# Performance work log

Hardware: AMD Instinct MI355X
Metric: run time of the kernel (lower is better)

Reference implementation:

```python
import jax, jax.numpy as jnp
import numpy as np

B, Q, K, H = 8, 512, 512, 64
KEY_D, QUERY_D, VAL_D = 256, 256, 256

def setup_inputs() -> dict:
    key = jax.random.key(0)
    ks = jax.random.split(key, 6)
    return {
        "key": jax.random.normal(ks[0], (B, K, KEY_D), dtype=jnp.float32),
        "query": jax.random.normal(ks[1], (B, Q, QUERY_D), dtype=jnp.float32),
        "value": jax.random.normal(ks[2], (B, K, VAL_D), dtype=jnp.float32),
        "mask": jnp.zeros((B, Q, K), dtype=bool),
        "W_k": jax.random.normal(ks[3], (KEY_D, H), dtype=jnp.float32) / np.sqrt(KEY_D),
        "W_q": jax.random.normal(ks[4], (QUERY_D, H), dtype=jnp.float32) / np.sqrt(QUERY_D),
        "w_v": jax.random.normal(ks[5], (H,), dtype=jnp.float32) / np.sqrt(H),
    }

def reference(key, query, value, mask, W_k, W_q, w_v):
    q = query @ W_q                      # [B, Q, H]
    k = key @ W_k                        # [B, K, H]
    feats = jnp.tanh(q[:, :, None, :] + k[:, None, :, :])  # [B, Q, K, H]
    score = jnp.einsum('bqkh,h->bqk', feats, w_v)           # [B, Q, K]
    score = jnp.where(mask, -jnp.inf, score)
    attn = jax.nn.softmax(score, axis=-1)                   # [B, Q, K]
    return jnp.einsum('bqk,bkd->bqd', attn, value)          # [B, Q, VAL_D]
```

## Files before the change

kernel.cpp:

```cpp
#include <hip/hip_runtime.h>
#include <math.h>

#define NB 8
#define NQ 512
#define NK 512
#define NH 64
#define ND 256
#define QT 8

typedef float f32x2 __attribute__((ext_vector_type(2)));
typedef float f32x4 __attribute__((ext_vector_type(4)));

#define EXP2(x) __builtin_amdgcn_exp2f(x)
#define RCP(x)  __builtin_amdgcn_rcpf(x)
#define SCALE2 2.8853900817779268f
#define LOG2E  1.4426950408889634f

static __device__ __forceinline__ f32x2 sp2(float v) { return (f32x2){v, v}; }
static __device__ __forceinline__ f32x2 fma2(f32x2 a, f32x2 b, f32x2 c) {
    return __builtin_elementwise_fma(a, b, c);
}
static __device__ __forceinline__ f32x2 mk2(float x, float y) {
    return (f32x2){x, y};
}

__global__ __launch_bounds__(256, 4) void proj_kernel(
    const float* __restrict__ query, const float* __restrict__ key,
    const float* __restrict__ Wq, const float* __restrict__ Wk,
    float* __restrict__ Eq, float* __restrict__ Ekp)
{
    __shared__ __align__(16) float insT[ND][12];
    __shared__ float pacc[3][4][NH][2];
    const int t = threadIdx.x;
    const bool isK = blockIdx.x >= 512;
    const float* __restrict__ in = isK ? key : query;
    const float* __restrict__ W  = isK ? Wk : Wq;
    const int rowbase = (blockIdx.x & 511) * 8;

    {
        const int r = t & 7, c = (t >> 3) * 8;
        const float* src = in + (size_t)(rowbase + r) * ND + c;
        const f32x4 v0 = *(const f32x4*)src;
        const f32x4 v1 = *(const f32x4*)(src + 4);
        insT[c + 0][r] = v0.x; insT[c + 1][r] = v0.y;
        insT[c + 2][r] = v0.z; insT[c + 3][r] = v0.w;
        insT[c + 4][r] = v1.x; insT[c + 5][r] = v1.y;
        insT[c + 6][r] = v1.z; insT[c + 7][r] = v1.w;
    }
    __syncthreads();

    const int lane = t & 63;
    const int w    = t >> 6;
    const int d0   = w * 64;

    f32x2 acc[4] = {{0.f,0.f},{0.f,0.f},{0.f,0.f},{0.f,0.f}};
    for (int dd = 0; dd < 64; ++dd) {
        const int d = d0 + dd;
        const float wv = W[(size_t)d * NH + lane];
        const f32x4 rA = *(const f32x4*)&insT[d][0];
        const f32x4 rB = *(const f32x4*)&insT[d][4];
        acc[0] = fma2(mk2(rA.x, rA.y), sp2(wv), acc[0]);
        acc[1] = fma2(mk2(rA.z, rA.w), sp2(wv), acc[1]);
        acc[2] = fma2(mk2(rB.x, rB.y), sp2(wv), acc[2]);
        acc[3] = fma2(mk2(rB.z, rB.w), sp2(wv), acc[3]);
    }
    if (w > 0) {
        #pragma unroll
        for (int rp = 0; rp < 4; ++rp)
            *(f32x2*)&pacc[w - 1][rp][lane][0] = acc[rp];
    }
    __syncthreads();
    if (w == 0) {
        float e[8];
        #pragma unroll
        for (int rp = 0; rp < 4; ++rp) {
            f32x2 a = acc[rp];
            a += *(const f32x2*)&pacc[0][rp][lane][0];
            a += *(const f32x2*)&pacc[1][rp][lane][0];
            a += *(const f32x2*)&pacc[2][rp][lane][0];
            e[2 * rp] = a.x; e[2 * rp + 1] = a.y;
        }
        #pragma unroll
        for (int j = 0; j < 8; ++j) {
            const float x = fminf(fmaxf(e[j] * SCALE2, -30.f), 30.f);
            e[j] = EXP2(x);
        }
        if (!isK) {
            #pragma unroll
            for (int j = 0; j < 8; ++j)
                Eq[(size_t)(rowbase + j) * NH + lane] = e[j];
        } else {
            #pragma unroll
            for (int j = 0; j < 8; ++j) {
                const int g = rowbase + j;
                const int bb = g >> 9, kk = g & 511;
                Ekp[((size_t)bb * NH + lane) * NK + kk] = e[j];
            }
        }
    }
}

__global__ __launch_bounds__(512, 4) void attn_kernel(
    const float* __restrict__ Eq, const float* __restrict__ Ekp,
    const float* __restrict__ value, const unsigned char* __restrict__ mask,
    const float* __restrict__ w_v, float* __restrict__ out)
{
    __shared__ __align__(16) float qT[NH][4][4];
    __shared__ float w01[32];
    __shared__ __align__(16) float ps[QT][NK];
    __shared__ __align__(16) float reds[QT][8];
    __shared__ __align__(16) float pacc[3][4][ND];

    const int t    = threadIdx.x;
    const int lane = t & 63;
    const int w    = t >> 6;
    const int b    = blockIdx.x >> 6;
    const int q0   = (blockIdx.x & 63) * QT;

    {
        const int r = w, h = lane;
        const float e = Eq[(size_t)(b * NQ + q0 + r) * NH + h];
        qT[h][r >> 1][r & 1]       = e;
        qT[h][r >> 1][2 + (r & 1)] = w_v[h ^ 1] * e;
    }
    if (t < 32) w01[t] = w_v[2 * t] + w_v[2 * t + 1];
    float wl = w_v[lane];
    #pragma unroll
    for (int off = 32; off; off >>= 1) wl += __shfl_xor(wl, off, 64);
    const float wsumL = wl * LOG2E;
    __syncthreads();

    const int k = (w << 6) + lane;
    const float* __restrict__ ekc = Ekp + (size_t)b * NH * NK + k;

    f32x2 acc[4] = {{0.f,0.f},{0.f,0.f},{0.f,0.f},{0.f,0.f}};
    float eka[4];
    #pragma unroll
    for (int j = 0; j < 4; ++j) eka[j] = ekc[(size_t)j * NK];

    for (int hc = 0; hc < 16; ++hc) {
        const float ek0 = eka[0], ek1 = eka[1], ek2 = eka[2], ek3 = eka[3];
        if (hc < 15) {
            #pragma unroll
            for (int j = 0; j < 4; ++j)
                eka[j] = ekc[(size_t)(4 * (hc + 1) + j) * NK];
        }
        const f32x2 w2 = *(const f32x2*)&w01[2 * hc];
        const int hb = 4 * hc;
        #pragma unroll
        for (int rp = 0; rp < 4; ++rp) {
            const f32x4 g0 = *(const f32x4*)&qT[hb + 0][rp][0];
            const f32x4 g1 = *(const f32x4*)&qT[hb + 1][rp][0];
            const f32x4 g2 = *(const f32x4*)&qT[hb + 2][rp][0];
            const f32x4 g3 = *(const f32x4*)&qT[hb + 3][rp][0];
            const f32x2 t0 = mk2(g0.x, g0.y) * ek0;
            const f32x2 t1 = mk2(g1.x, g1.y) * ek1;
            const f32x2 ua = t0 + t1 + 1.0f;
            const f32x2 da = fma2(t0, t1, ua);
            f32x2 na = fma2(mk2(g0.z, g0.w), sp2(ek0), sp2(w2.x));
            na = fma2(mk2(g1.z, g1.w), sp2(ek1), na);
            const f32x2 t2 = mk2(g2.x, g2.y) * ek2;
            const f32x2 t3 = mk2(g3.x, g3.y) * ek3;
            const f32x2 ub = t2 + t3 + 1.0f;
            const f32x2 db = fma2(t2, t3, ub);
            f32x2 nb = fma2(mk2(g2.z, g2.w), sp2(ek2), sp2(w2.y));
            nb = fma2(mk2(g3.z, g3.w), sp2(ek3), nb);
            const f32x2 D = da * db;
            f32x2 N = na * db;
            N = fma2(nb, da, N);
            const f32x2 rD = mk2(RCP(D.x), RCP(D.y));
            acc[rp] = fma2(N, rD, acc[rp]);
        }
    }

    float p[8];
    {
        const unsigned char* __restrict__ mb =
            mask + (size_t)(b * NQ + q0) * NK + k;
        #pragma unroll
        for (int rp = 0; rp < 4; ++rp) {
            const f32x2 arg = fma2(acc[rp], sp2(-2.f * LOG2E), sp2(wsumL));
            p[2 * rp]     = mb[(size_t)(2 * rp) * NK]     ? -__builtin_inff() : arg.x;
            p[2 * rp + 1] = mb[(size_t)(2 * rp + 1) * NK] ? -__builtin_inff() : arg.y;
        }
        #pragma unroll
        for (int r = 0; r < 8; ++r) p[r] = EXP2(p[r]);
    }

    #pragma unroll
    for (int r = 0; r < 8; ++r) {
        float s = p[r];
        #pragma unroll
        for (int off = 32; off; off >>= 1) s += __shfl_xor(s, off, 64);
        if (lane == 0) reds[r][w] = s;
    }
    __syncthreads();
    #pragma unroll
    for (int r = 0; r < 8; ++r) {
        const f32x4 sa = *(const f32x4*)&reds[r][0];
        const f32x4 sb = *(const f32x4*)&reds[r][4];
        const float gsum = ((sa.x + sa.y) + (sa.z + sa.w)) +
                           ((sb.x + sb.y) + (sb.z + sb.w));
        ps[r][k] = p[r] * RCP(gsum);
    }
    __syncthreads();

    const int kq   = w >> 1;
    const int dh   = w & 1;
    const int dcol = dh * 128 + 2 * lane;
    f32x2 a[QT];
    #pragma unroll
    for (int r = 0; r < QT; ++r) a[r] = (f32x2){0.f, 0.f};

    const float* __restrict__ vb = value + ((size_t)b * NK + kq * 128) * ND + dcol;
    for (int kk = 0; kk < 128; kk += 4) {
        const int kbase = kq * 128 + kk;
        const f32x2 v0 = *(const f32x2*)&vb[(size_t)(kk + 0) * ND];
        const f32x2 v1 = *(const f32x2*)&vb[(size_t)(kk + 1) * ND];
        const f32x2 v2 = *(const f32x2*)&vb[(size_t)(kk + 2) * ND];
        const f32x2 v3 = *(const f32x2*)&vb[(size_t)(kk + 3) * ND];
        #pragma unroll
        for (int half = 0; half < 2; ++half) {
            #pragma unroll
            for (int rr = 0; rr < 4; ++rr) {
                const int r = half * 4 + rr;
                const f32x4 P = *(const f32x4*)&ps[r][kbase];
                a[r] = fma2(sp2(P.x), v0, a[r]);
                a[r] = fma2(sp2(P.y), v1, a[r]);
                a[r] = fma2(sp2(P.z), v2, a[r]);
                a[r] = fma2(sp2(P.w), v3, a[r]);
            }
        }
    }

    if (kq > 0) {
        #pragma unroll
        for (int r = 0; r < 4; ++r)
            *(f32x2*)&pacc[kq - 1][r][dcol] = a[r];
    }
    __syncthreads();
    if (kq == 0) {
        #pragma unroll
        for (int r = 0; r < 4; ++r) {
            f32x2 v = a[r];
            v += *(const f32x2*)&pacc[0][r][dcol];
            v += *(const f32x2*)&pacc[1][r][dcol];
            v += *(const f32x2*)&pacc[2][r][dcol];
            *(f32x2*)&out[(size_t)(b * NQ + q0 + r) * ND + dcol] = v;
        }
    }
    __syncthreads();
    if (kq > 0) {
        #pragma unroll
        for (int r = 0; r < 4; ++r)
            *(f32x2*)&pacc[kq - 1][r][dcol] = a[4 + r];
    }
    __syncthreads();
    if (kq == 0) {
        #pragma unroll
        for (int r = 0; r < 4; ++r) {
            f32x2 v = a[4 + r];
            v += *(const f32x2*)&pacc[0][r][dcol];
            v += *(const f32x2*)&pacc[1][r][dcol];
            v += *(const f32x2*)&pacc[2][r][dcol];
            *(f32x2*)&out[(size_t)(b * NQ + q0 + 4 + r) * ND + dcol] = v;
        }
    }
}

extern "C" void kernel_launch(void* const* d_in, const int* in_sizes, int n_in,
                              void* d_out, int out_size, void* d_ws, size_t ws_size,
                              hipStream_t stream) {
    const float* key   = (const float*)d_in[0];
    const float* query = (const float*)d_in[1];
    const float* value = (const float*)d_in[2];
    const unsigned char* mask = (const unsigned char*)d_in[3];
    const float* Wk  = (const float*)d_in[4];
    const float* Wq  = (const float*)d_in[5];
    const float* w_v = (const float*)d_in[6];
    float* out = (float*)d_out;

    float* Eq  = (float*)d_ws;
    float* Ekp = Eq + (size_t)NB * NQ * NH;

    proj_kernel<<<1024, 256, 0, stream>>>(query, key, Wq, Wk, Eq, Ekp);
    attn_kernel<<<NB * (NQ / QT), 512, 0, stream>>>(Eq, Ekp, value, mask, w_v, out);
}
```

Measured before the change: 48.59 us.

## Precompute q-side operands in proj kernel and remap attn score work to 2k×4q per thread

The projection kernel now writes the query-side factors (exp values and their w_v-scaled copies) in a packed per-row layout, plus the pairwise w_v sums and the total w_v sum to global memory. This removes the shared-memory staging, the first barrier and the reduction from the attention kernel. In the attention kernel each thread now scores two keys for four query rows, reading q operands straight from global/L1 as vector loads with double-buffered key prefetch. Block IDs are swizzled across batches. This trades LDS traffic and a sync for more global reads and register pressure.

```diff
diff --git a/kernel.cpp b/kernel.cpp
--- a/kernel.cpp
+++ b/kernel.cpp
@@ -24,10 +24,36 @@
     return (f32x2){x, y};
 }
 
+static __device__ __forceinline__ void score4(
+    const f32x2 k0, const f32x2 k1, const f32x2 k2, const f32x2 k3,
+    const f32x4 eqv, const f32x4 fqv, const float w01a, const float w01b,
+    f32x2& acc)
+{
+    const f32x2 t0 = k0 * eqv.x;
+    const f32x2 t1 = k1 * eqv.y;
+    const f32x2 ua = t0 + t1 + 1.0f;
+    const f32x2 da = fma2(t0, t1, ua);
+    f32x2 na = fma2(k0, sp2(fqv.x), sp2(w01a));
+    na = fma2(k1, sp2(fqv.y), na);
+    const f32x2 t2 = k2 * eqv.z;
+    const f32x2 t3 = k3 * eqv.w;
+    const f32x2 ub = t2 + t3 + 1.0f;
+    const f32x2 db = fma2(t2, t3, ub);
+    f32x2 nb = fma2(k2, sp2(fqv.z), sp2(w01b));
+    nb = fma2(k3, sp2(fqv.w), nb);
+    const f32x2 D = da * db;
+    f32x2 N = na * db;
+    N = fma2(nb, da, N);
+    const f32x2 rD = mk2(RCP(D.x), RCP(D.y));
+    acc = fma2(N, rD, acc);
+}
+
 __global__ __launch_bounds__(256, 4) void proj_kernel(
     const float* __restrict__ query, const float* __restrict__ key,
     const float* __restrict__ Wq, const float* __restrict__ Wk,
-    float* __restrict__ Eq, float* __restrict__ Ekp)
+    const float* __restrict__ w_v,
+    float* __restrict__ qside, float* __restrict__ Ekp,
+    float* __restrict__ w01g, float* __restrict__ wsumg)
 {
     __shared__ __align__(16) float insT[ND][12];
     __shared__ float pacc[3][4][NH][2];
@@ -86,9 +112,14 @@
             e[j] = EXP2(x);
         }
         if (!isK) {
-            #pragma unroll
-            for (int j = 0; j < 8; ++j)
-                Eq[(size_t)(rowbase + j) * NH + lane] = e[j];
+            const float wx = w_v[lane ^ 1];
+            #pragma unroll
+            for (int j = 0; j < 8; ++j) {
+                const int g = rowbase + j;
+                float* dst = qside + ((size_t)g * 16 + (lane >> 2)) * 8 + (lane & 3);
+                dst[0] = e[j];
+                dst[4] = wx * e[j];
+            }
         } else {
             #pragma unroll
             for (int j = 0; j < 8; ++j) {
@@ -98,110 +129,106 @@
             }
         }
     }
+    if (blockIdx.x == 0) {
+        if (t < 32) w01g[t] = w_v[2 * t] + w_v[2 * t + 1];
+        if (t == 64) {
+            float s = 0.f;
+            for (int h = 0; h < NH; ++h) s += w_v[h];
+            wsumg[0] = s;
+        }
+    }
 }
 
 __global__ __launch_bounds__(512, 4) void attn_kernel(
-    const float* __restrict__ Eq, const float* __restrict__ Ekp,
+    const float* __restrict__ qside, const float* __restrict__ Ekp,
     const float* __restrict__ value, const unsigned char* __restrict__ mask,
-    const float* __restrict__ w_v, float* __restrict__ out)
+    const float* __restrict__ w01g, const float* __restrict__ wsumg,
+    float* __restrict__ out)
 {
-    __shared__ __align__(16) float qT[NH][4][4];
-    __shared__ float w01[32];
     __shared__ __align__(16) float ps[QT][NK];
-    __shared__ __align__(16) float reds[QT][8];
+    __shared__ __align__(16) float reds[QT][4];
     __shared__ __align__(16) float pacc[3][4][ND];
 
     const int t    = threadIdx.x;
     const int lane = t & 63;
     const int w    = t >> 6;
-    const int b    = blockIdx.x >> 6;
-    const int q0   = (blockIdx.x & 63) * QT;
-
-    {
-        const int r = w, h = lane;
-        const float e = Eq[(size_t)(b * NQ + q0 + r) * NH + h];
-        qT[h][r >> 1][r & 1]       = e;
-        qT[h][r >> 1][2 + (r & 1)] = w_v[h ^ 1] * e;
-    }
-    if (t < 32) w01[t] = w_v[2 * t] + w_v[2 * t + 1];
-    float wl = w_v[lane];
-    #pragma unroll
-    for (int off = 32; off; off >>= 1) wl += __shfl_xor(wl, off, 64);
-    const float wsumL = wl * LOG2E;
-    __syncthreads();
-
-    const int k = (w << 6) + lane;
-    const float* __restrict__ ekc = Ekp + (size_t)b * NH * NK + k;
+    const int bid  = ((int)(blockIdx.x & 7) << 6) | ((int)blockIdx.x >> 3);
+    const int b    = bid >> 6;
+    const int q0   = (bid & 63) * QT;
+    const int rh   = __builtin_amdgcn_readfirstlane(t >> 8);
+    const int kp   = t & 255;
+
+    const float wsumL = wsumg[0] * LOG2E;
+    const float* __restrict__ qs  = qside + (size_t)(b * NQ + q0 + rh * 4) * 128;
+    const float* __restrict__ ekc = Ekp + (size_t)b * NH * NK + 2 * kp;
+
+    f32x2 eA[4], eB[4];
+    #pragma unroll
+    for (int j = 0; j < 4; ++j) eA[j] = *(const f32x2*)&ekc[(size_t)j * NK];
+    #pragma unroll
+    for (int j = 0; j < 4; ++j) eB[j] = *(const f32x2*)&ekc[(size_t)(4 + j) * NK];
 
     f32x2 acc[4] = {{0.f,0.f},{0.f,0.f},{0.f,0.f},{0.f,0.f}};
-    float eka[4];
-    #pragma unroll
-    for (int j = 0; j < 4; ++j) eka[j] = ekc[(size_t)j * NK];
-
-    for (int hc = 0; hc < 16; ++hc) {
-        const float ek0 = eka[0], ek1 = eka[1], ek2 = eka[2], ek3 = eka[3];
-        if (hc < 15) {
-            #pragma unroll
-            for (int j = 0; j < 4; ++j)
-                eka[j] = ekc[(size_t)(4 * (hc + 1) + j) * NK];
-        }
-        const f32x2 w2 = *(const f32x2*)&w01[2 * hc];
-        const int hb = 4 * hc;
-        #pragma unroll
-        for (int rp = 0; rp < 4; ++rp) {
-            const f32x4 g0 = *(const f32x4*)&qT[hb + 0][rp][0];
-            const f32x4 g1 = *(const f32x4*)&qT[hb + 1][rp][0];
-            const f32x4 g2 = *(const f32x4*)&qT[hb + 2][rp][0];
-            const f32x4 g3 = *(const f32x4*)&qT[hb + 3][rp][0];
-            const f32x2 t0 = mk2(g0.x, g0.y) * ek0;
-            const f32x2 t1 = mk2(g1.x, g1.y) * ek1;
-            const f32x2 ua = t0 + t1 + 1.0f;
-            const f32x2 da = fma2(t0, t1, ua);
-            f32x2 na = fma2(mk2(g0.z, g0.w), sp2(ek0), sp2(w2.x));
-            na = fma2(mk2(g1.z, g1.w), sp2(ek1), na);
-            const f32x2 t2 = mk2(g2.x, g2.y) * ek2;
-            const f32x2 t3 = mk2(g3.x, g3.y) * ek3;
-            const f32x2 ub = t2 + t3 + 1.0f;
-            const f32x2 db = fma2(t2, t3, ub);
-            f32x2 nb = fma2(mk2(g2.z, g2.w), sp2(ek2), sp2(w2.y));
-            nb = fma2(mk2(g3.z, g3.w), sp2(ek3), nb);
-            const f32x2 D = da * db;
-            f32x2 N = na * db;
-            N = fma2(nb, da, N);
-            const f32x2 rD = mk2(RCP(D.x), RCP(D.y));
-            acc[rp] = fma2(N, rD, acc[rp]);
-        }
-    }
-
-    float p[8];
-    {
-        const unsigned char* __restrict__ mb =
-            mask + (size_t)(b * NQ + q0) * NK + k;
-        #pragma unroll
-        for (int rp = 0; rp < 4; ++rp) {
-            const f32x2 arg = fma2(acc[rp], sp2(-2.f * LOG2E), sp2(wsumL));
-            p[2 * rp]     = mb[(size_t)(2 * rp) * NK]     ? -__builtin_inff() : arg.x;
-            p[2 * rp + 1] = mb[(size_t)(2 * rp + 1) * NK] ? -__builtin_inff() : arg.y;
-        }
-        #pragma unroll
-        for (int r = 0; r < 8; ++r) p[r] = EXP2(p[r]);
-    }
-
-    #pragma unroll
-    for (int r = 0; r < 8; ++r) {
-        float s = p[r];
+
+    for (int hc = 0; hc < 16; hc += 2) {
+        {
+            const f32x2 k0 = eA[0], k1 = eA[1], k2 = eA[2], k3 = eA[3];
+            if (hc + 2 < 16) {
+                #pragma unroll
+                for (int j = 0; j < 4; ++j)
+                    eA[j] = *(const f32x2*)&ekc[(size_t)(4 * (hc + 2) + j) * NK];
+            }
+            const float wa = w01g[2 * hc], wb = w01g[2 * hc + 1];
+            #pragma unroll
+            for (int r = 0; r < 4; ++r) {
+                const f32x4 eqv = *(const f32x4*)&qs[r * 128 + hc * 8];
+                const f32x4 fqv = *(const f32x4*)&qs[r * 128 + hc * 8 + 4];
+                score4(k0, k1, k2, k3, eqv, fqv, wa, wb, acc[r]);
+            }
+        }
+        {
+            const f32x2 k0 = eB[0], k1 = eB[1], k2 = eB[2], k3 = eB[3];
+            if (hc + 3 < 16) {
+                #pragma unroll
+                for (int j = 0; j < 4; ++j)
+                    eB[j] = *(const f32x2*)&ekc[(size_t)(4 * (hc + 3) + j) * NK];
+            }
+            const float wa = w01g[2 * hc + 2], wb = w01g[2 * hc + 3];
+            #pragma unroll
+            for (int r = 0; r < 4; ++r) {
+                const f32x4 eqv = *(const f32x4*)&qs[r * 128 + (hc + 1) * 8];
+                const f32x4 fqv = *(const f32x4*)&qs[r * 128 + (hc + 1) * 8 + 4];
+                score4(k0, k1, k2, k3, eqv, fqv, wa, wb, acc[r]);
+            }
+        }
+    }
+
+    const unsigned char* __restrict__ mb =
+        mask + (size_t)(b * NQ + q0 + rh * 4) * NK + 2 * kp;
+    f32x2 p[4];
+    #pragma unroll
+    for (int r = 0; r < 4; ++r) {
+        f32x2 arg = fma2(acc[r], sp2(-2.f * LOG2E), sp2(wsumL));
+        const unsigned short m = *(const unsigned short*)(mb + (size_t)r * NK);
+        if (m & 0x00ff) arg.x = -__builtin_inff();
+        if (m & 0xff00) arg.y = -__builtin_inff();
+        p[r] = mk2(EXP2(arg.x), EXP2(arg.y));
+    }
+
+    #pragma unroll
+    for (int r = 0; r < 4; ++r) {
+        float s = p[r].x + p[r].y;
         #pragma unroll
         for (int off = 32; off; off >>= 1) s += __shfl_xor(s, off, 64);
-        if (lane == 0) reds[r][w] = s;
-    }
-    __syncthreads();
-    #pragma unroll
-    for (int r = 0; r < 8; ++r) {
-        const f32x4 sa = *(const f32x4*)&reds[r][0];
-        const f32x4 sb = *(const f32x4*)&reds[r][4];
-        const float gsum = ((sa.x + sa.y) + (sa.z + sa.w)) +
-                           ((sb.x + sb.y) + (sb.z + sb.w));
-        ps[r][k] = p[r] * RCP(gsum);
+        if (lane == 0) reds[rh * 4 + r][w & 3] = s;
+    }
+    __syncthreads();
+    #pragma unroll
+    for (int r = 0; r < 4; ++r) {
+        const f32x4 sv = *(const f32x4*)&reds[rh * 4 + r][0];
+        const float gsum = (sv.x + sv.y) + (sv.z + sv.w);
+        p[r] = p[r] * RCP(gsum);
+        *(f32x2*)&ps[rh * 4 + r][2 * kp] = p[r];
     }
     __syncthreads();
 
@@ -280,9 +307,13 @@
     const float* w_v = (const float*)d_in[6];
     float* out = (float*)d_out;
 
-    float* Eq  = (float*)d_ws;
-    float* Ekp = Eq + (size_t)NB * NQ * NH;
-
-    proj_kernel<<<1024, 256, 0, stream>>>(query, key, Wq, Wk, Eq, Ekp);
-    attn_kernel<<<NB * (NQ / QT), 512, 0, stream>>>(Eq, Ekp, value, mask, w_v, out);
-}
+    float* Ekp   = (float*)d_ws;
+    float* qside = Ekp + (size_t)NB * NH * NK;
+    float* w01g  = qside + (size_t)NB * NQ * 128;
+    float* wsumg = w01g + 32;
+
+    proj_kernel<<<1024, 256, 0, stream>>>(query, key, Wq, Wk, w_v,
+                                          qside, Ekp, w01g, wsumg);
+    attn_kernel<<<NB * (NQ / QT), 512, 0, stream>>>(qside, Ekp, value, mask,
+                                                    w01g, wsumg, out);
+}
```

After: 48.25 us. About the same (-0.7%).
